# Kernel tuning notes

Measured on AMD Instinct MI355X. Metric: run time of the kernel, lower is better.

## Reference

```python
import jax, jax.numpy as jnp
import numpy as np
from jax import lax

TOP_K = 4
N_GROUP = 4
TOPK_GROUP = 2
ROUTED_SCALE = 2.5
NEG_INF = -1e9


def setup_inputs() -> dict:
    key = jax.random.key(0)
    ks = jax.random.split(key, 6)
    B, S, H, I, E = 2, 2048, 1024, 512, 16
    x = jax.random.normal(ks[0], (B, S, H), dtype=jnp.float32)
    router_weight = jax.random.normal(ks[1], (E, H), dtype=jnp.float32) * 0.02
    router_bias = jnp.zeros((E,), dtype=jnp.float32)
    w_gate = jax.random.normal(ks[2], (E, I, H), dtype=jnp.float32) * 0.02
    w_up = jax.random.normal(ks[3], (E, I, H), dtype=jnp.float32) * 0.02
    w_down = jax.random.normal(ks[4], (E, H, I), dtype=jnp.float32) * 0.02
    return {"x": x, "router_weight": router_weight, "router_bias": router_bias,
            "w_gate": w_gate, "w_up": w_up, "w_down": w_down}


def _route(xf, router_weight, router_bias):
    # DeepSeek-V3 sigmoid router with group-limited top-k.
    T = xf.shape[0]
    E = router_weight.shape[0]
    logits = xf @ router_weight.T                      # [T, E]
    scores = jax.nn.sigmoid(logits)                    # [T, E]
    s_choice = scores + router_bias                    # bias used only for selection
    per_group = E // N_GROUP
    sg = s_choice.reshape(T, N_GROUP, per_group)
    group_scores = lax.top_k(sg, 2)[0].sum(-1)         # [T, n_group] sum of top-2
    _, gidx = lax.top_k(group_scores, TOPK_GROUP)      # [T, topk_group]
    gmask = jnp.zeros((T, N_GROUP), dtype=bool).at[jnp.arange(T)[:, None], gidx].set(True)
    masked = jnp.where(gmask[:, :, None], sg, NEG_INF).reshape(T, E)
    _, topk_idx = lax.top_k(masked, TOP_K)             # [T, top_k]
    w = jnp.take_along_axis(scores, topk_idx, axis=1)  # original sigmoid scores
    w = w / (w.sum(-1, keepdims=True) + 1e-20) * ROUTED_SCALE
    combine = jnp.zeros((T, E), dtype=xf.dtype).at[jnp.arange(T)[:, None], topk_idx].add(w)
    return combine


def reference(x, router_weight, router_bias, w_gate, w_up, w_down):
    B, S, H = x.shape
    E = w_gate.shape[0]
    xf = x.reshape(-1, H)                              # [T, H]
    combine = _route(xf, router_weight, router_bias)   # [T, E]
    # Grouped-GEMM SwiGLU experts expressed as per-expert dense GEMMs with
    # combine-weighted accumulation (same math as sort+grouped-mm+scatter).
    out = jnp.zeros_like(xf)
    for e in range(E):
        g = xf @ w_gate[e].T                           # [T, I]
        u = xf @ w_up[e].T                             # [T, I]
        y_e = (jax.nn.silu(g) * u) @ w_down[e].T       # [T, H]
        out = out + combine[:, e:e + 1] * y_e
    return out.reshape(B, S, H)
```

## Files before the change

### kernel.cpp

```cpp
#include <hip/hip_runtime.h>
#include <stdint.h>

#define T_TOK   4096
#define H_DIM   1024
#define I_DIM   512
#define E_EXP   16
#define TOPK    4
#define NTILEMAX 144

typedef __attribute__((ext_vector_type(8))) short bf16x8;
typedef __attribute__((ext_vector_type(4))) float f32x4;
typedef __attribute__((ext_vector_type(8))) unsigned short ushort8;

__device__ __forceinline__ unsigned short f2bf(float f) {
  unsigned u = __float_as_uint(f);
  u = u + 0x7fffu + ((u >> 16) & 1u);
  return (unsigned short)(u >> 16);
}
__device__ __forceinline__ float bf2f(unsigned short s) {
  return __uint_as_float(((unsigned)s) << 16);
}

__device__ __forceinline__ void gload_lds16(const void* g, void* l) {
  __builtin_amdgcn_global_load_lds(
      (const __attribute__((address_space(1))) unsigned int*)g,
      (__attribute__((address_space(3))) unsigned int*)l, 16, 0, 0);
}

__device__ __forceinline__ void cvt_seg8(const float* __restrict__ src,
                                         unsigned short* __restrict__ dst,
                                         int n8, int tid0, int stride) {
  for (int i = tid0; i < n8; i += stride) {
    float4 v0 = ((const float4*)src)[2 * i];
    float4 v1 = ((const float4*)src)[2 * i + 1];
    ushort8 o;
    o[0] = f2bf(v0.x); o[1] = f2bf(v0.y); o[2] = f2bf(v0.z); o[3] = f2bf(v0.w);
    o[4] = f2bf(v1.x); o[5] = f2bf(v1.y); o[6] = f2bf(v1.z); o[7] = f2bf(v1.w);
    ((ushort8*)dst)[i] = o;
  }
}

__global__ __launch_bounds__(256) void cvt_w_kernel(
    const float* __restrict__ wg, unsigned short* __restrict__ wgb,
    const float* __restrict__ wu, unsigned short* __restrict__ wub,
    const float* __restrict__ wd, unsigned short* __restrict__ wdb) {
  const int tid0 = blockIdx.x * blockDim.x + threadIdx.x;
  const int stride = gridDim.x * blockDim.x;
  cvt_seg8(wg, wgb, E_EXP * I_DIM * H_DIM / 8, tid0, stride);
  cvt_seg8(wu, wub, E_EXP * I_DIM * H_DIM / 8, tid0, stride);
  cvt_seg8(wd, wdb, E_EXP * H_DIM * I_DIM / 8, tid0, stride);
}

__global__ __launch_bounds__(256) void logits_kernel(
    const float* __restrict__ x, const float* __restrict__ rw,
    float* __restrict__ logits, unsigned short* __restrict__ xb) {
  const int t = blockIdx.x * 4 + (threadIdx.x >> 6);
  const int lane = threadIdx.x & 63;
  const float* xr = x + (size_t)t * H_DIM;

  float4 xv[4];
#pragma unroll
  for (int i = 0; i < 4; ++i) xv[i] = ((const float4*)xr)[i * 64 + lane];

  unsigned short* xrow = xb + (size_t)t * H_DIM;
#pragma unroll
  for (int i = 0; i < 4; ++i) {
    ushort4 o;
    o.x = f2bf(xv[i].x); o.y = f2bf(xv[i].y);
    o.z = f2bf(xv[i].z); o.w = f2bf(xv[i].w);
    ((ushort4*)xrow)[i * 64 + lane] = o;
  }

#pragma unroll
  for (int g = 0; g < 4; ++g) {
    float acc[4] = {0.f, 0.f, 0.f, 0.f};
#pragma unroll
    for (int e4 = 0; e4 < 4; ++e4) {
      const float* wrow = rw + (size_t)(g * 4 + e4) * H_DIM;
#pragma unroll
      for (int i = 0; i < 4; ++i) {
        float4 wv = ((const float4*)wrow)[i * 64 + lane];
        acc[e4] = fmaf(xv[i].x, wv.x, acc[e4]);
        acc[e4] = fmaf(xv[i].y, wv.y, acc[e4]);
        acc[e4] = fmaf(xv[i].z, wv.z, acc[e4]);
        acc[e4] = fmaf(xv[i].w, wv.w, acc[e4]);
      }
    }
#pragma unroll
    for (int e4 = 0; e4 < 4; ++e4)
#pragma unroll
      for (int off = 32; off > 0; off >>= 1) acc[e4] += __shfl_down(acc[e4], off, 64);
    if (lane == 0)
      ((float4*)(logits + (size_t)t * E_EXP))[g] =
          make_float4(acc[0], acc[1], acc[2], acc[3]);
  }
}

__global__ __launch_bounds__(256) void select_kernel(
    const float* __restrict__ logits, const float* __restrict__ rb,
    int* __restrict__ tidx, float* __restrict__ tw) {
  const int t = blockIdx.x * 256 + threadIdx.x;

  float sc[E_EXP], sch[E_EXP];
#pragma unroll
  for (int e = 0; e < E_EXP; ++e) {
    sc[e] = 1.f / (1.f + expf(-logits[(size_t)t * E_EXP + e]));
    sch[e] = sc[e] + rb[e];
  }

  float gsum[4];
#pragma unroll
  for (int g = 0; g < 4; ++g) {
    float m1 = -3e38f, m2 = -3e38f;
#pragma unroll
    for (int j = 0; j < 4; ++j) {
      float v = sch[g * 4 + j];
      if (v > m1) { m2 = m1; m1 = v; } else if (v > m2) { m2 = v; }
    }
    gsum[g] = m1 + m2;
  }
  int g1 = 0;
  for (int g = 1; g < 4; ++g) if (gsum[g] > gsum[g1]) g1 = g;
  int g2 = -1;
  for (int g = 0; g < 4; ++g)
    if (g != g1 && (g2 < 0 || gsum[g] > gsum[g2])) g2 = g;

  float cand[E_EXP];
#pragma unroll
  for (int e = 0; e < E_EXP; ++e)
    cand[e] = ((e >> 2) == g1 || (e >> 2) == g2) ? sch[e] : -1e9f;

  int idx[TOPK]; float wv[TOPK]; float wsum = 0.f;
#pragma unroll
  for (int k = 0; k < TOPK; ++k) {
    int bi = 0; float bv = cand[0];
#pragma unroll
    for (int e = 1; e < E_EXP; ++e) if (cand[e] > bv) { bv = cand[e]; bi = e; }
    idx[k] = bi; cand[bi] = -3e38f;
    wv[k] = sc[bi];
    wsum += wv[k];
  }
  float scale = 2.5f / (wsum + 1e-20f);
#pragma unroll
  for (int k = 0; k < TOPK; ++k) {
    tidx[t * 4 + k] = idx[k];
    tw[t * 4 + k] = wv[k] * scale;
  }
}

__global__ __launch_bounds__(256) void count_kernel(
    const int* __restrict__ tidx, int* __restrict__ counts) {
  const int e = blockIdx.x, tid = threadIdx.x;
  const int lane = tid & 63, wv = tid >> 6;
  int local = 0;
  for (int i = tid; i < T_TOK * TOPK; i += 256) local += (tidx[i] == e);
#pragma unroll
  for (int off = 32; off > 0; off >>= 1) local += __shfl_down(local, off, 64);
  __shared__ int ws[4];
  if (lane == 0) ws[wv] = local;
  __syncthreads();
  if (tid == 0) counts[e] = ws[0] + ws[1] + ws[2] + ws[3];
}

__global__ void prefix_kernel(const int* __restrict__ counts,
                              int* __restrict__ off, int* __restrict__ toff) {
  if (threadIdx.x == 0) {
    int a = 0, tt = 0;
    for (int e = 0; e < E_EXP; ++e) {
      off[e] = a; toff[e] = tt;
      a += counts[e];
      tt += (counts[e] + 127) >> 7;
    }
    off[E_EXP] = a;
    toff[E_EXP] = tt;
  }
}

__global__ __launch_bounds__(256) void scatter_kernel(
    const int* __restrict__ tidx, const int* __restrict__ off,
    int* __restrict__ rowmap, int* __restrict__ rowtok) {
  const int e = blockIdx.x, tid = threadIdx.x;
  const int lane = tid & 63, wv = tid >> 6;
  __shared__ int wsum[4];
  __shared__ int srun;
  if (tid == 0) srun = 0;
  __syncthreads();
  const int base = off[e];
  for (int c = 0; c < T_TOK * TOPK / 256; ++c) {
    const int i = c * 256 + tid;
    const bool f = (tidx[i] == e);
    unsigned long long m = __ballot(f);
    int wpre = __popcll(m & ((1ull << lane) - 1ull));
    if (lane == 63) wsum[wv] = wpre + (f ? 1 : 0);
    __syncthreads();
    const int run = srun;
    int pre = 0, tot = 0;
#pragma unroll
    for (int w = 0; w < 4; ++w) {
      int v = wsum[w];
      if (w < wv) pre += v;
      tot += v;
    }
    if (f) {
      const int pos = base + run + pre + wpre;
      rowmap[i] = pos;
      rowtok[pos] = i >> 2;
    }
    __syncthreads();
    if (tid == 0) srun = run + tot;
  }
}

__device__ __forceinline__ int find_expert(const int* __restrict__ toff, int tile) {
  int e = 0;
#pragma unroll
  for (int q = 1; q <= E_EXP; ++q) e += (toff[q] <= tile);
  return e;
}

__global__ __launch_bounds__(256, 3) void gateup_kernel(
    const unsigned short* __restrict__ xbf,
    const unsigned short* __restrict__ wgbf,
    const unsigned short* __restrict__ wubf,
    const int* __restrict__ rowtok, const int* __restrict__ off,
    const int* __restrict__ toff,
    unsigned short* __restrict__ hbuf) {
  const int bid = (int)blockIdx.x;
  const int work = (bid & 7) * NTILEMAX + (bid >> 3);
  const int tile = work >> 3, tn = work & 7;
  if (tile >= toff[E_EXP]) return;
  const int e = find_expert(toff, tile);
  const int tm = tile - toff[e];
  const int seg0 = off[e];
  const int nrows = off[e + 1] - seg0;

  __shared__ __align__(16) unsigned short As[128 * 64];
  __shared__ __align__(16) unsigned short Gs[64 * 64];
  __shared__ __align__(16) unsigned short Us[64 * 64];
  __shared__ int ids[128];

  const int tid = threadIdx.x;
  if (tid < 128) {
    int r = tm * 128 + tid;
    ids[tid] = rowtok[seg0 + (r < nrows ? r : 0)];
  }
  __syncthreads();

  const int col8 = tid & 7;
  const int r0 = tid >> 3;
  const int csrc = (col8 ^ (r0 & 7)) * 8;
  int tokA[4];
#pragma unroll
  for (int j = 0; j < 4; ++j) tokA[j] = ids[j * 32 + r0];

  const unsigned short* wg = wgbf + (size_t)e * I_DIM * H_DIM + (size_t)(tn * 64) * H_DIM;
  const unsigned short* wu = wubf + (size_t)e * I_DIM * H_DIM + (size_t)(tn * 64) * H_DIM;

  f32x4 accg[4][2], accu[4][2];
#pragma unroll
  for (int m = 0; m < 4; ++m)
#pragma unroll
    for (int n = 0; n < 2; ++n) { accg[m][n] = (f32x4)0.f; accu[m][n] = (f32x4)0.f; }

  const int lane = tid & 63, wid = tid >> 6;
  const int wr = wid >> 1, wc = wid & 1;
  const int frow = lane & 15, fr7 = frow & 7;
  const int kc = lane >> 4;

  for (int kt = 0; kt < H_DIM / 64; ++kt) {
    const int kb = kt * 64 + csrc;
    __syncthreads();
#pragma unroll
    for (int j = 0; j < 4; ++j)
      gload_lds16(xbf + ((size_t)tokA[j] * H_DIM + kb), (char*)As + (j * 256 + tid) * 16);
#pragma unroll
    for (int j = 0; j < 2; ++j) {
      gload_lds16(wg + ((size_t)(j * 32 + r0) * H_DIM + kb), (char*)Gs + (j * 256 + tid) * 16);
      gload_lds16(wu + ((size_t)(j * 32 + r0) * H_DIM + kb), (char*)Us + (j * 256 + tid) * 16);
    }
    __syncthreads();
#pragma unroll
    for (int kk = 0; kk < 2; ++kk) {
      const int swz = ((kk * 4 + kc) ^ fr7) * 8;
      bf16x8 af[4], bg[2], bu[2];
#pragma unroll
      for (int m = 0; m < 4; ++m)
        af[m] = *(const bf16x8*)&As[(wr * 64 + m * 16 + frow) * 64 + swz];
#pragma unroll
      for (int n = 0; n < 2; ++n) {
        bg[n] = *(const bf16x8*)&Gs[(wc * 32 + n * 16 + frow) * 64 + swz];
        bu[n] = *(const bf16x8*)&Us[(wc * 32 + n * 16 + frow) * 64 + swz];
      }
#pragma unroll
      for (int m = 0; m < 4; ++m)
#pragma unroll
        for (int n = 0; n < 2; ++n) {
          accg[m][n] = __builtin_amdgcn_mfma_f32_16x16x32_bf16(af[m], bg[n], accg[m][n], 0, 0, 0);
          accu[m][n] = __builtin_amdgcn_mfma_f32_16x16x32_bf16(af[m], bu[n], accu[m][n], 0, 0, 0);
        }
    }
  }

  const int lr = (lane >> 4) * 4, lc = lane & 15;
#pragma unroll
  for (int m = 0; m < 4; ++m) {
#pragma unroll
    for (int j = 0; j < 4; ++j) {
      int r = tm * 128 + wr * 64 + m * 16 + lr + j;
      if (r < nrows) {
        size_t rowoff = (size_t)(seg0 + r) * I_DIM;
#pragma unroll
        for (int n = 0; n < 2; ++n) {
          float g = accg[m][n][j];
          float u = accu[m][n][j];
          float hv = g / (1.f + __expf(-g)) * u;
          hbuf[rowoff + tn * 64 + wc * 32 + n * 16 + lc] = f2bf(hv);
        }
      }
    }
  }
}

__global__ __launch_bounds__(256, 3) void down_kernel(
    const unsigned short* __restrict__ hbuf,
    const unsigned short* __restrict__ wdbf,
    const int* __restrict__ off, const int* __restrict__ toff,
    unsigned short* __restrict__ ybuf) {
  const int bid = (int)blockIdx.x;
  const int work = (bid & 7) * NTILEMAX + (bid >> 3);
  const int tile = work >> 3, tn = work & 7;
  if (tile >= toff[E_EXP]) return;
  const int e = find_expert(toff, tile);
  const int tm = tile - toff[e];
  const int seg0 = off[e];
  const int nrows = off[e + 1] - seg0;

  __shared__ __align__(16) unsigned short As[128 * 64];
  __shared__ __align__(16) unsigned short Bs[128 * 64];

  const int tid = threadIdx.x;
  const int col8 = tid & 7;
  const int r0 = tid >> 3;
  const int csrc = (col8 ^ (r0 & 7)) * 8;
  int rowA[4];
#pragma unroll
  for (int j = 0; j < 4; ++j) {
    int r = tm * 128 + j * 32 + r0;
    rowA[j] = seg0 + (r < nrows ? r : nrows - 1);
  }
  const unsigned short* wd = wdbf + (size_t)e * H_DIM * I_DIM + (size_t)(tn * 128) * I_DIM;

  f32x4 acc[4][4];
#pragma unroll
  for (int m = 0; m < 4; ++m)
#pragma unroll
    for (int n = 0; n < 4; ++n) acc[m][n] = (f32x4)0.f;

  const int lane = tid & 63, wid = tid >> 6;
  const int wr = wid >> 1, wc = wid & 1;
  const int frow = lane & 15, fr7 = frow & 7;
  const int kc = lane >> 4;

  for (int kt = 0; kt < I_DIM / 64; ++kt) {
    const int kb = kt * 64 + csrc;
    __syncthreads();
#pragma unroll
    for (int j = 0; j < 4; ++j) {
      gload_lds16(hbuf + ((size_t)rowA[j] * I_DIM + kb), (char*)As + (j * 256 + tid) * 16);
      gload_lds16(wd + ((size_t)(j * 32 + r0) * I_DIM + kb), (char*)Bs + (j * 256 + tid) * 16);
    }
    __syncthreads();
#pragma unroll
    for (int kk = 0; kk < 2; ++kk) {
      const int swz = ((kk * 4 + kc) ^ fr7) * 8;
      bf16x8 af[4], bw[4];
#pragma unroll
      for (int m = 0; m < 4; ++m)
        af[m] = *(const bf16x8*)&As[(wr * 64 + m * 16 + frow) * 64 + swz];
#pragma unroll
      for (int n = 0; n < 4; ++n)
        bw[n] = *(const bf16x8*)&Bs[(wc * 64 + n * 16 + frow) * 64 + swz];
#pragma unroll
      for (int m = 0; m < 4; ++m)
#pragma unroll
        for (int n = 0; n < 4; ++n)
          acc[m][n] = __builtin_amdgcn_mfma_f32_16x16x32_bf16(af[m], bw[n], acc[m][n], 0, 0, 0);
    }
  }

  const int lr = (lane >> 4) * 4, lc = lane & 15;
#pragma unroll
  for (int m = 0; m < 4; ++m) {
#pragma unroll
    for (int j = 0; j < 4; ++j) {
      int r = tm * 128 + wr * 64 + m * 16 + lr + j;
      if (r < nrows) {
        size_t rowoff = (size_t)(seg0 + r) * H_DIM;
#pragma unroll
        for (int n = 0; n < 4; ++n)
          ybuf[rowoff + tn * 128 + wc * 64 + n * 16 + lc] = f2bf(acc[m][n][j]);
      }
    }
  }
}

__global__ __launch_bounds__(256) void combine_kernel(
    const unsigned short* __restrict__ ybuf, const int* __restrict__ rowmap,
    const float* __restrict__ tw, float* __restrict__ out) {
  int t = blockIdx.x, tid = threadIdx.x;
  __shared__ int rloc[4];
  __shared__ float wloc[4];
  if (tid < 4) { rloc[tid] = rowmap[t * 4 + tid]; wloc[tid] = tw[t * 4 + tid]; }
  __syncthreads();
  int c = tid * 4;
  float4 a = {0.f, 0.f, 0.f, 0.f};
#pragma unroll
  for (int k = 0; k < 4; ++k) {
    ushort4 v = *(const ushort4*)&ybuf[(size_t)rloc[k] * H_DIM + c];
    float w = wloc[k];
    a.x += w * bf2f(v.x); a.y += w * bf2f(v.y);
    a.z += w * bf2f(v.z); a.w += w * bf2f(v.w);
  }
  *(float4*)&out[(size_t)t * H_DIM + c] = a;
}

extern "C" void kernel_launch(void* const* d_in, const int* in_sizes, int n_in,
                              void* d_out, int out_size, void* d_ws, size_t ws_size,
                              hipStream_t stream) {
  (void)in_sizes; (void)n_in; (void)out_size; (void)ws_size;
  const float* x  = (const float*)d_in[0];
  const float* rw = (const float*)d_in[1];
  const float* rb = (const float*)d_in[2];
  const float* wg = (const float*)d_in[3];
  const float* wu = (const float*)d_in[4];
  const float* wd = (const float*)d_in[5];
  float* out = (float*)d_out;

  char* base = (char*)d_ws;
  size_t o = 0;
  auto alloc = [&](size_t b) -> void* {
    void* p = base + o;
    o += (b + 255) & ~(size_t)255;
    return p;
  };
  unsigned short* xbf   = (unsigned short*)alloc((size_t)T_TOK * H_DIM * 2);
  unsigned short* wgbf  = (unsigned short*)alloc((size_t)E_EXP * I_DIM * H_DIM * 2);
  unsigned short* wubf  = (unsigned short*)alloc((size_t)E_EXP * I_DIM * H_DIM * 2);
  unsigned short* wdbf  = (unsigned short*)alloc((size_t)E_EXP * H_DIM * I_DIM * 2);
  unsigned short* hbuf  = (unsigned short*)alloc((size_t)T_TOK * TOPK * I_DIM * 2);
  unsigned short* ybuf  = (unsigned short*)alloc((size_t)T_TOK * TOPK * H_DIM * 2);
  float* logits = (float*)alloc((size_t)T_TOK * E_EXP * 4);
  int*   tidx   = (int*)alloc((size_t)T_TOK * TOPK * 4);
  float* tw     = (float*)alloc((size_t)T_TOK * TOPK * 4);
  int*   rowmap = (int*)alloc((size_t)T_TOK * TOPK * 4);
  int*   rowtok = (int*)alloc((size_t)T_TOK * TOPK * 4);
  int*   counts = (int*)alloc(256);
  int*   offb   = (int*)alloc(256);
  int*   toffb  = (int*)alloc(256);

  cvt_w_kernel<<<2048, 256, 0, stream>>>(wg, wgbf, wu, wubf, wd, wdbf);

  logits_kernel<<<T_TOK / 4, 256, 0, stream>>>(x, rw, logits, xbf);
  select_kernel<<<T_TOK / 256, 256, 0, stream>>>(logits, rb, tidx, tw);
  count_kernel<<<E_EXP, 256, 0, stream>>>(tidx, counts);
  prefix_kernel<<<1, 64, 0, stream>>>(counts, offb, toffb);
  scatter_kernel<<<E_EXP, 256, 0, stream>>>(tidx, offb, rowmap, rowtok);

  gateup_kernel<<<8 * NTILEMAX, 256, 0, stream>>>(xbf, wgbf, wubf, rowtok, offb, toffb, hbuf);
  down_kernel<<<8 * NTILEMAX, 256, 0, stream>>>(hbuf, wdbf, offb, toffb, ybuf);
  combine_kernel<<<T_TOK, 256, 0, stream>>>(ybuf, rowmap, tw, out);
}
```

Baseline: 157.7 us.

## Fuse fp32-to-bf16 weight conversion into expert GEMM tile loads

Removes the separate weight conversion kernel. The gate/up and down GEMMs now read fp32 weights directly, convert them to bf16 in registers with packed convert instructions, and store them into swizzled LDS. This drops one full fp32 read plus a bf16 write and re-read of all expert weights. In exchange, each GEMM tile now reads twice as many weight bytes, weights are re-read per M-tile, and the B loads become synchronous register loads instead of async global-to-LDS loads.

After: 156.4 us. About the same (-0.9%).

```diff
diff --git a/kernel.cpp b/kernel.cpp
--- a/kernel.cpp
+++ b/kernel.cpp
@@ -21,34 +21,16 @@
   return __uint_as_float(((unsigned)s) << 16);
 }
 
+__device__ __forceinline__ unsigned cvtpk(float lo, float hi) {
+  unsigned r;
+  asm("v_cvt_pk_bf16_f32 %0, %1, %2" : "=v"(r) : "v"(lo), "v"(hi));
+  return r;
+}
+
 __device__ __forceinline__ void gload_lds16(const void* g, void* l) {
   __builtin_amdgcn_global_load_lds(
       (const __attribute__((address_space(1))) unsigned int*)g,
       (__attribute__((address_space(3))) unsigned int*)l, 16, 0, 0);
-}
-
-__device__ __forceinline__ void cvt_seg8(const float* __restrict__ src,
-                                         unsigned short* __restrict__ dst,
-                                         int n8, int tid0, int stride) {
-  for (int i = tid0; i < n8; i += stride) {
-    float4 v0 = ((const float4*)src)[2 * i];
-    float4 v1 = ((const float4*)src)[2 * i + 1];
-    ushort8 o;
-    o[0] = f2bf(v0.x); o[1] = f2bf(v0.y); o[2] = f2bf(v0.z); o[3] = f2bf(v0.w);
-    o[4] = f2bf(v1.x); o[5] = f2bf(v1.y); o[6] = f2bf(v1.z); o[7] = f2bf(v1.w);
-    ((ushort8*)dst)[i] = o;
-  }
-}
-
-__global__ __launch_bounds__(256) void cvt_w_kernel(
-    const float* __restrict__ wg, unsigned short* __restrict__ wgb,
-    const float* __restrict__ wu, unsigned short* __restrict__ wub,
-    const float* __restrict__ wd, unsigned short* __restrict__ wdb) {
-  const int tid0 = blockIdx.x * blockDim.x + threadIdx.x;
-  const int stride = gridDim.x * blockDim.x;
-  cvt_seg8(wg, wgb, E_EXP * I_DIM * H_DIM / 8, tid0, stride);
-  cvt_seg8(wu, wub, E_EXP * I_DIM * H_DIM / 8, tid0, stride);
-  cvt_seg8(wd, wdb, E_EXP * H_DIM * I_DIM / 8, tid0, stride);
 }
 
 __global__ __launch_bounds__(256) void logits_kernel(
@@ -220,8 +202,8 @@
 
 __global__ __launch_bounds__(256, 3) void gateup_kernel(
     const unsigned short* __restrict__ xbf,
-    const unsigned short* __restrict__ wgbf,
-    const unsigned short* __restrict__ wubf,
+    const float* __restrict__ wgf,
+    const float* __restrict__ wuf,
     const int* __restrict__ rowtok, const int* __restrict__ off,
     const int* __restrict__ toff,
     unsigned short* __restrict__ hbuf) {
@@ -249,12 +231,14 @@
   const int col8 = tid & 7;
   const int r0 = tid >> 3;
   const int csrc = (col8 ^ (r0 & 7)) * 8;
+  const int bcol = col8 * 8;
+  const int bdst = (col8 ^ (r0 & 7)) * 8;
   int tokA[4];
 #pragma unroll
   for (int j = 0; j < 4; ++j) tokA[j] = ids[j * 32 + r0];
 
-  const unsigned short* wg = wgbf + (size_t)e * I_DIM * H_DIM + (size_t)(tn * 64) * H_DIM;
-  const unsigned short* wu = wubf + (size_t)e * I_DIM * H_DIM + (size_t)(tn * 64) * H_DIM;
+  const float* wg = wgf + (size_t)e * I_DIM * H_DIM + (size_t)(tn * 64) * H_DIM;
+  const float* wu = wuf + (size_t)e * I_DIM * H_DIM + (size_t)(tn * 64) * H_DIM;
 
   f32x4 accg[4][2], accu[4][2];
 #pragma unroll
@@ -268,15 +252,26 @@
   const int kc = lane >> 4;
 
   for (int kt = 0; kt < H_DIM / 64; ++kt) {
-    const int kb = kt * 64 + csrc;
+    const int kbA = kt * 64 + csrc;
+    const int kbB = kt * 64 + bcol;
     __syncthreads();
 #pragma unroll
     for (int j = 0; j < 4; ++j)
-      gload_lds16(xbf + ((size_t)tokA[j] * H_DIM + kb), (char*)As + (j * 256 + tid) * 16);
+      gload_lds16(xbf + ((size_t)tokA[j] * H_DIM + kbA), (char*)As + (j * 256 + tid) * 16);
 #pragma unroll
     for (int j = 0; j < 2; ++j) {
-      gload_lds16(wg + ((size_t)(j * 32 + r0) * H_DIM + kb), (char*)Gs + (j * 256 + tid) * 16);
-      gload_lds16(wu + ((size_t)(j * 32 + r0) * H_DIM + kb), (char*)Us + (j * 256 + tid) * 16);
+      const int row = j * 32 + r0;
+      const float4* gs = (const float4*)(wg + (size_t)row * H_DIM + kbB);
+      const float4* us = (const float4*)(wu + (size_t)row * H_DIM + kbB);
+      float4 g0 = gs[0], g1 = gs[1];
+      float4 u0 = us[0], u1 = us[1];
+      uint4 gw, uw;
+      gw.x = cvtpk(g0.x, g0.y); gw.y = cvtpk(g0.z, g0.w);
+      gw.z = cvtpk(g1.x, g1.y); gw.w = cvtpk(g1.z, g1.w);
+      uw.x = cvtpk(u0.x, u0.y); uw.y = cvtpk(u0.z, u0.w);
+      uw.z = cvtpk(u1.x, u1.y); uw.w = cvtpk(u1.z, u1.w);
+      *(uint4*)&Gs[row * 64 + bdst] = gw;
+      *(uint4*)&Us[row * 64 + bdst] = uw;
     }
     __syncthreads();
 #pragma unroll
@@ -323,7 +318,7 @@
 
 __global__ __launch_bounds__(256, 3) void down_kernel(
     const unsigned short* __restrict__ hbuf,
-    const unsigned short* __restrict__ wdbf,
+    const float* __restrict__ wdf,
     const int* __restrict__ off, const int* __restrict__ toff,
     unsigned short* __restrict__ ybuf) {
   const int bid = (int)blockIdx.x;
@@ -342,13 +337,15 @@
   const int col8 = tid & 7;
   const int r0 = tid >> 3;
   const int csrc = (col8 ^ (r0 & 7)) * 8;
+  const int bcol = col8 * 8;
+  const int bdst = (col8 ^ (r0 & 7)) * 8;
   int rowA[4];
 #pragma unroll
   for (int j = 0; j < 4; ++j) {
     int r = tm * 128 + j * 32 + r0;
     rowA[j] = seg0 + (r < nrows ? r : nrows - 1);
   }
-  const unsigned short* wd = wdbf + (size_t)e * H_DIM * I_DIM + (size_t)(tn * 128) * I_DIM;
+  const float* wd = wdf + (size_t)e * H_DIM * I_DIM + (size_t)(tn * 128) * I_DIM;
 
   f32x4 acc[4][4];
 #pragma unroll
@@ -362,12 +359,21 @@
   const int kc = lane >> 4;
 
   for (int kt = 0; kt < I_DIM / 64; ++kt) {
-    const int kb = kt * 64 + csrc;
-    __syncthreads();
+    const int kbA = kt * 64 + csrc;
+    const int kbB = kt * 64 + bcol;
+    __syncthreads();
+#pragma unroll
+    for (int j = 0; j < 4; ++j)
+      gload_lds16(hbuf + ((size_t)rowA[j] * I_DIM + kbA), (char*)As + (j * 256 + tid) * 16);
 #pragma unroll
     for (int j = 0; j < 4; ++j) {
-      gload_lds16(hbuf + ((size_t)rowA[j] * I_DIM + kb), (char*)As + (j * 256 + tid) * 16);
-      gload_lds16(wd + ((size_t)(j * 32 + r0) * I_DIM + kb), (char*)Bs + (j * 256 + tid) * 16);
+      const int row = j * 32 + r0;
+      const float4* ds = (const float4*)(wd + (size_t)row * I_DIM + kbB);
+      float4 d0 = ds[0], d1 = ds[1];
+      uint4 w;
+      w.x = cvtpk(d0.x, d0.y); w.y = cvtpk(d0.z, d0.w);
+      w.z = cvtpk(d1.x, d1.y); w.w = cvtpk(d1.z, d1.w);
+      *(uint4*)&Bs[row * 64 + bdst] = w;
     }
     __syncthreads();
 #pragma unroll
@@ -444,9 +450,6 @@
     return p;
   };
   unsigned short* xbf   = (unsigned short*)alloc((size_t)T_TOK * H_DIM * 2);
-  unsigned short* wgbf  = (unsigned short*)alloc((size_t)E_EXP * I_DIM * H_DIM * 2);
-  unsigned short* wubf  = (unsigned short*)alloc((size_t)E_EXP * I_DIM * H_DIM * 2);
-  unsigned short* wdbf  = (unsigned short*)alloc((size_t)E_EXP * H_DIM * I_DIM * 2);
   unsigned short* hbuf  = (unsigned short*)alloc((size_t)T_TOK * TOPK * I_DIM * 2);
   unsigned short* ybuf  = (unsigned short*)alloc((size_t)T_TOK * TOPK * H_DIM * 2);
   float* logits = (float*)alloc((size_t)T_TOK * E_EXP * 4);
@@ -458,15 +461,13 @@
   int*   offb   = (int*)alloc(256);
   int*   toffb  = (int*)alloc(256);
 
-  cvt_w_kernel<<<2048, 256, 0, stream>>>(wg, wgbf, wu, wubf, wd, wdbf);
-
   logits_kernel<<<T_TOK / 4, 256, 0, stream>>>(x, rw, logits, xbf);
   select_kernel<<<T_TOK / 256, 256, 0, stream>>>(logits, rb, tidx, tw);
   count_kernel<<<E_EXP, 256, 0, stream>>>(tidx, counts);
   prefix_kernel<<<1, 64, 0, stream>>>(counts, offb, toffb);
   scatter_kernel<<<E_EXP, 256, 0, stream>>>(tidx, offb, rowmap, rowtok);
 
-  gateup_kernel<<<8 * NTILEMAX, 256, 0, stream>>>(xbf, wgbf, wubf, rowtok, offb, toffb, hbuf);
-  down_kernel<<<8 * NTILEMAX, 256, 0, stream>>>(hbuf, wdbf, offb, toffb, ybuf);
+  gateup_kernel<<<8 * NTILEMAX, 256, 0, stream>>>(xbf, wg, wu, rowtok, offb, toffb, hbuf);
+  down_kernel<<<8 * NTILEMAX, 256, 0, stream>>>(hbuf, wd, offb, toffb, ybuf);
   combine_kernel<<<T_TOK, 256, 0, stream>>>(ybuf, rowmap, tw, out);
 }
```

## Fuse router logits with top-k selection and merge count/prefix/scatter kernels

Applied to the files above, without the earlier changes.

Expert selection is folded into the logits kernel: lane 0 of each wave runs the sigmoid, group-limited top-k and weight normalisation directly on the reduced logits, so the logits buffer and the separate select launch are no longer needed. The count, prefix and scatter kernels are merged into one plan kernel. Each of its blocks builds the full expert histogram with shared-memory atomics, block 0 writes the offsets, and every block computes its own base before scattering. This removes three launches and their global round trips. The cost is redundant histogramming in all 16 blocks and serial selection work on one lane per wave.

New measurement: 163.8 us. +3.9%, slower.

```diff
diff --git a/kernel.cpp b/kernel.cpp
--- a/kernel.cpp
+++ b/kernel.cpp
@@ -51,9 +51,10 @@
   cvt_seg8(wd, wdb, E_EXP * H_DIM * I_DIM / 8, tid0, stride);
 }
 
-__global__ __launch_bounds__(256) void logits_kernel(
+__global__ __launch_bounds__(256) void logits_sel_kernel(
     const float* __restrict__ x, const float* __restrict__ rw,
-    float* __restrict__ logits, unsigned short* __restrict__ xb) {
+    const float* __restrict__ rb, unsigned short* __restrict__ xb,
+    int* __restrict__ tidx, float* __restrict__ tw) {
   const int t = blockIdx.x * 4 + (threadIdx.x >> 6);
   const int lane = threadIdx.x & 63;
   const float* xr = x + (size_t)t * H_DIM;
@@ -71,6 +72,7 @@
     ((ushort4*)xrow)[i * 64 + lane] = o;
   }
 
+  float myl[E_EXP];
 #pragma unroll
   for (int g = 0; g < 4; ++g) {
     float acc[4] = {0.f, 0.f, 0.f, 0.f};
@@ -87,24 +89,18 @@
       }
     }
 #pragma unroll
-    for (int e4 = 0; e4 < 4; ++e4)
+    for (int e4 = 0; e4 < 4; ++e4) {
 #pragma unroll
       for (int off = 32; off > 0; off >>= 1) acc[e4] += __shfl_down(acc[e4], off, 64);
-    if (lane == 0)
-      ((float4*)(logits + (size_t)t * E_EXP))[g] =
-          make_float4(acc[0], acc[1], acc[2], acc[3]);
-  }
-}
-
-__global__ __launch_bounds__(256) void select_kernel(
-    const float* __restrict__ logits, const float* __restrict__ rb,
-    int* __restrict__ tidx, float* __restrict__ tw) {
-  const int t = blockIdx.x * 256 + threadIdx.x;
+      myl[g * 4 + e4] = acc[e4];
+    }
+  }
+  if (lane != 0) return;
 
   float sc[E_EXP], sch[E_EXP];
 #pragma unroll
   for (int e = 0; e < E_EXP; ++e) {
-    sc[e] = 1.f / (1.f + expf(-logits[(size_t)t * E_EXP + e]));
+    sc[e] = 1.f / (1.f + expf(-myl[e]));
     sch[e] = sc[e] + rb[e];
   }
 
@@ -148,44 +144,34 @@
   }
 }
 
-__global__ __launch_bounds__(256) void count_kernel(
-    const int* __restrict__ tidx, int* __restrict__ counts) {
+__global__ __launch_bounds__(256) void plan_kernel(
+    const int* __restrict__ tidx, int* __restrict__ offg,
+    int* __restrict__ toffg, int* __restrict__ rowmap,
+    int* __restrict__ rowtok) {
   const int e = blockIdx.x, tid = threadIdx.x;
   const int lane = tid & 63, wv = tid >> 6;
-  int local = 0;
-  for (int i = tid; i < T_TOK * TOPK; i += 256) local += (tidx[i] == e);
-#pragma unroll
-  for (int off = 32; off > 0; off >>= 1) local += __shfl_down(local, off, 64);
-  __shared__ int ws[4];
-  if (lane == 0) ws[wv] = local;
-  __syncthreads();
-  if (tid == 0) counts[e] = ws[0] + ws[1] + ws[2] + ws[3];
-}
-
-__global__ void prefix_kernel(const int* __restrict__ counts,
-                              int* __restrict__ off, int* __restrict__ toff) {
-  if (threadIdx.x == 0) {
-    int a = 0, tt = 0;
-    for (int e = 0; e < E_EXP; ++e) {
-      off[e] = a; toff[e] = tt;
-      a += counts[e];
-      tt += (counts[e] + 127) >> 7;
-    }
-    off[E_EXP] = a;
-    toff[E_EXP] = tt;
-  }
-}
-
-__global__ __launch_bounds__(256) void scatter_kernel(
-    const int* __restrict__ tidx, const int* __restrict__ off,
-    int* __restrict__ rowmap, int* __restrict__ rowtok) {
-  const int e = blockIdx.x, tid = threadIdx.x;
-  const int lane = tid & 63, wv = tid >> 6;
+  __shared__ int histo[E_EXP];
   __shared__ int wsum[4];
   __shared__ int srun;
+  if (tid < E_EXP) histo[tid] = 0;
   if (tid == 0) srun = 0;
   __syncthreads();
-  const int base = off[e];
+  for (int i = tid; i < T_TOK * TOPK; i += 256)
+    atomicAdd(&histo[tidx[i]], 1);
+  __syncthreads();
+
+  if (e == 0 && tid == 0) {
+    int a = 0, tt = 0;
+    for (int q = 0; q < E_EXP; ++q) {
+      offg[q] = a; toffg[q] = tt;
+      a += histo[q];
+      tt += (histo[q] + 127) >> 7;
+    }
+    offg[E_EXP] = a; toffg[E_EXP] = tt;
+  }
+  int base = 0;
+  for (int q = 0; q < e; ++q) base += histo[q];
+
   for (int c = 0; c < T_TOK * TOPK / 256; ++c) {
     const int i = c * 256 + tid;
     const bool f = (tidx[i] == e);
@@ -449,22 +435,17 @@
   unsigned short* wdbf  = (unsigned short*)alloc((size_t)E_EXP * H_DIM * I_DIM * 2);
   unsigned short* hbuf  = (unsigned short*)alloc((size_t)T_TOK * TOPK * I_DIM * 2);
   unsigned short* ybuf  = (unsigned short*)alloc((size_t)T_TOK * TOPK * H_DIM * 2);
-  float* logits = (float*)alloc((size_t)T_TOK * E_EXP * 4);
   int*   tidx   = (int*)alloc((size_t)T_TOK * TOPK * 4);
   float* tw     = (float*)alloc((size_t)T_TOK * TOPK * 4);
   int*   rowmap = (int*)alloc((size_t)T_TOK * TOPK * 4);
   int*   rowtok = (int*)alloc((size_t)T_TOK * TOPK * 4);
-  int*   counts = (int*)alloc(256);
   int*   offb   = (int*)alloc(256);
   int*   toffb  = (int*)alloc(256);
 
   cvt_w_kernel<<<2048, 256, 0, stream>>>(wg, wgbf, wu, wubf, wd, wdbf);
 
-  logits_kernel<<<T_TOK / 4, 256, 0, stream>>>(x, rw, logits, xbf);
-  select_kernel<<<T_TOK / 256, 256, 0, stream>>>(logits, rb, tidx, tw);
-  count_kernel<<<E_EXP, 256, 0, stream>>>(tidx, counts);
-  prefix_kernel<<<1, 64, 0, stream>>>(counts, offb, toffb);
-  scatter_kernel<<<E_EXP, 256, 0, stream>>>(tidx, offb, rowmap, rowtok);
+  logits_sel_kernel<<<T_TOK / 4, 256, 0, stream>>>(x, rw, rb, xbf, tidx, tw);
+  plan_kernel<<<E_EXP, 256, 0, stream>>>(tidx, offb, toffb, rowmap, rowtok);
 
   gateup_kernel<<<8 * NTILEMAX, 256, 0, stream>>>(xbf, wgbf, wubf, rowtok, offb, toffb, hbuf);
   down_kernel<<<8 * NTILEMAX, 256, 0, stream>>>(hbuf, wdbf, offb, toffb, ybuf);
```
